# Kernel tuning notes

Measured on AMD Instinct MI355X. Metric: run time of the kernel, lower is better.

Reference implementation:

```python
import jax, jax.numpy as jnp
import numpy as np
import math

N_EMBD = 1024
N_HEAD = 16
N_LAYER = 12


def setup_inputs() -> dict:
    key = jax.random.key(0)
    kx, kw, kb = jax.random.split(key, 3)
    B, T, C = 4, 2048, N_EMBD
    x = jax.random.normal(kx, (B, T, C), dtype=jnp.float32)
    # nn.Linear(C, 3C): weight [3C, C] scaled by 1/sqrt(2*n_layer), bias [3C]
    bound = 1.0 / math.sqrt(C)
    W = jax.random.uniform(kw, (3 * C, C), minval=-bound, maxval=bound, dtype=jnp.float32)
    W = W * (1.0 / math.sqrt(N_LAYER * 2))
    b = jax.random.uniform(kb, (3 * C,), minval=-bound, maxval=bound, dtype=jnp.float32)
    return {"x": x, "W": W, "b": b}


def reference(x, W, b) -> jnp.ndarray:
    B, T, C = x.shape
    H = N_HEAD
    D = C // H
    qkv = jnp.einsum("btc,oc->bto", x, W) + b  # [B, T, 3C]
    q, k, v = jnp.split(qkv, 3, axis=-1)
    # [B, H, T, D]
    q = q.reshape(B, T, H, D).transpose(0, 2, 1, 3)
    k = k.reshape(B, T, H, D).transpose(0, 2, 1, 3)
    v = v.reshape(B, T, H, D).transpose(0, 2, 1, 3)
    att = jnp.einsum("bhtd,bhsd->bhts", q, k) / math.sqrt(D)  # [B, H, T, T]
    causal = jnp.tril(jnp.ones((T, T), dtype=bool))
    att = jnp.where(causal, att, -jnp.inf)
    att = jax.nn.softmax(att, axis=-1)
    y = jnp.einsum("bhts,bhsd->bhtd", att, v)  # [B, H, T, D]
    return y.transpose(0, 2, 1, 3).reshape(B, T, C)
```

## Files before the change

kernel.cpp:

```cpp
#include <hip/hip_runtime.h>


typedef __attribute__((ext_vector_type(8))) short short8;
typedef __attribute__((ext_vector_type(4))) short s16x4;
typedef __attribute__((ext_vector_type(4))) float f32x4;

#define AS1 __attribute__((address_space(1)))
#define AS3 __attribute__((address_space(3)))

__device__ __forceinline__ unsigned short f2bf(float f) {
  unsigned int u = __float_as_uint(f);
  u += 0x7fffu + ((u >> 16) & 1u);
  return (unsigned short)(u >> 16);
}

__device__ __forceinline__ unsigned int pack_bf16(float lo, float hi) {
  return __builtin_amdgcn_perm(__float_as_uint(hi) + 0x8000u,
                               __float_as_uint(lo) + 0x8000u, 0x07060302u);
}

__device__ __forceinline__ void async_copy16(const unsigned short* g, unsigned short* l) {
  const AS1 unsigned char* gp = (const AS1 unsigned char*)(unsigned long long)(uintptr_t)g;
  AS3 unsigned char* lp = (AS3 unsigned char*)(unsigned int)(uintptr_t)l;
  __builtin_amdgcn_global_load_lds((const AS1 void*)gp, (AS3 void*)lp, 16, 0, 0);
}

__global__ __launch_bounds__(256) void cvt_both(const float* __restrict__ x,
                                                const float* __restrict__ W,
                                                unsigned short* __restrict__ xt,
                                                unsigned short* __restrict__ wt) {
  int U = blockIdx.x * 256 + threadIdx.x;
  const float* in;
  unsigned short* out;
  if (U < 1048576) { in = x; out = xt; }
  else             { in = W; out = wt; U -= 1048576; }
  int u6 = U & 63, frag = (U >> 6) & 15, kt = (U >> 10) & 15, bt = U >> 14;
  int ks = frag & 1, i = (frag >> 1) & 3, half = frag >> 3;
  int row = bt * 128 + half * 64 + i * 16 + (u6 & 15);
  int colf = kt * 64 + ks * 32 + (u6 >> 4) * 8;
  const float4* p = (const float4*)(in + (size_t)row * 1024 + colf);
  float4 a = p[0], b = p[1];
  uint4 o;
  o.x = pack_bf16(a.x, a.y);
  o.y = pack_bf16(a.z, a.w);
  o.z = pack_bf16(b.x, b.y);
  o.w = pack_bf16(b.z, b.w);
  *(uint4*)(out + (size_t)U * 8) = o;
}

__global__ __launch_bounds__(256) void qkv_gemm(const unsigned short* __restrict__ xt,
                                                const unsigned short* __restrict__ wt,
                                                const float* __restrict__ bias,
                                                unsigned short* __restrict__ qb,
                                                unsigned short* __restrict__ kvb) {
  __shared__ unsigned short As[2][4096];
  __shared__ unsigned short Bs[2][4096];
  int tid = threadIdx.x;
  int wave = tid >> 6, lane = tid & 63;
  int q4 = lane >> 4, l16 = lane & 15;
  int bm = blockIdx.x, bn = blockIdx.y;

  f32x4 zero = {0.f, 0.f, 0.f, 0.f};
  f32x4 acc[4][4];
#pragma unroll
  for (int i = 0; i < 4; ++i)
#pragma unroll
    for (int j = 0; j < 4; ++j) acc[i][j] = zero;

  const unsigned short* Abase = xt + (size_t)bm * 16 * 8192;
  const unsigned short* Bbase = wt + (size_t)bn * 16 * 8192;

  auto stage = [&](int d, int kt32) {
    int kt64 = kt32 >> 1, ks = kt32 & 1;
    const unsigned short* ga = Abase + (size_t)kt64 * 8192;
    const unsigned short* gb = Bbase + (size_t)kt64 * 8192;
#pragma unroll
    for (int j = 0; j < 2; ++j) {
      int fi = wave * 2 + j;
      int f = (fi >> 2) * 8 + (fi & 3) * 2 + ks;
      async_copy16(ga + f * 512 + lane * 8, &As[d][fi * 512]);
      async_copy16(gb + f * 512 + lane * 8, &Bs[d][fi * 512]);
    }
  };

  stage(0, 0);
  for (int kt = 0; kt < 32; ++kt) {
    __syncthreads();
    if (kt < 31) stage((kt + 1) & 1, kt + 1);
    const unsigned short* Ac = As[kt & 1];
    const unsigned short* Bc = Bs[kt & 1];
    short8 af[4], bf[4];
#pragma unroll
    for (int i = 0; i < 4; ++i)
      af[i] = *(const short8*)(Ac + ((wave & 1) * 4 + i) * 512 + lane * 8);
#pragma unroll
    for (int j = 0; j < 4; ++j)
      bf[j] = *(const short8*)(Bc + ((wave >> 1) * 4 + j) * 512 + lane * 8);
#pragma unroll
    for (int i = 0; i < 4; ++i)
#pragma unroll
      for (int j = 0; j < 4; ++j)
        acc[i][j] = __builtin_amdgcn_mfma_f32_16x16x32_bf16(af[i], bf[j], acc[i][j], 0, 0, 0);
  }

  const float QSCALE = 0.18033688011112042f;
  int rowbase = bm * 128 + (wave & 1) * 64;
  int colbase = bn * 128 + (wave >> 1) * 64;
#pragma unroll
  for (int j = 0; j < 4; ++j) {
    int o = colbase + j * 16 + l16;
    float bv = bias[o];
#pragma unroll
    for (int i = 0; i < 4; ++i) {
      int r0 = rowbase + i * 16 + q4 * 4;
      int b = r0 >> 11, t0 = r0 & 2047;
      if (o < 1024) {
        int h = o >> 6, d = o & 63;
#pragma unroll
        for (int r = 0; r < 4; ++r)
          qb[((((size_t)b * 16 + h) * 2048 + t0 + r) << 6) + d] =
              f2bf((acc[i][j][r] + bv) * QSCALE);
      } else if (o < 2048) {
        int o2 = o - 1024;
        int h = o2 >> 6, dd = o2 & 63;
        int st = t0 >> 6, s6 = t0 & 63;
        int ns = s6 >> 4, l16p = s6 & 15;
        int ks = dd >> 5, q4p = (dd & 31) >> 3, jj = dd & 7;
        size_t base = ((size_t)(b * 16 + h) * 32 + st) * 8192 +
                      ((ns * 2 + ks) * 64 + q4p * 16 + l16p) * 8 + jj;
#pragma unroll
        for (int r = 0; r < 4; ++r)
          kvb[base + r * 8] = f2bf(acc[i][j][r] + bv);
      } else {
        int o3 = o - 2048;
        int h = o3 >> 6, dd = o3 & 63;
        int st = t0 >> 6, s6 = t0 & 63;
        int ns = s6 >> 4, q4p = (s6 >> 2) & 3;
        int p = dd >> 5, halfd = (dd >> 4) & 1, l16p = dd & 15;
        size_t base = ((size_t)(b * 16 + h) * 32 + st) * 8192 + 4096 +
                      ((ns * 2 + p) * 64 + q4p * 16 + l16p) * 8 + halfd * 4;
        ushort4 pk;
        pk.x = f2bf(acc[i][j][0] + bv);
        pk.y = f2bf(acc[i][j][1] + bv);
        pk.z = f2bf(acc[i][j][2] + bv);
        pk.w = f2bf(acc[i][j][3] + bv);
        *(ushort4*)(&kvb[base]) = pk;
      }
    }
  }
}

__global__ __launch_bounds__(128, 4) void flash_attn(const unsigned short* __restrict__ qb,
                                                     const unsigned short* __restrict__ kvb,
                                                     float* __restrict__ out) {
  __shared__ unsigned short buf[2][8192];

  const int tid = threadIdx.x;
  const int wave = tid >> 6, lane = tid & 63;
  const int q4 = lane >> 4, l16 = lane & 15;
  const int n = blockIdx.x;
  const int bh = (n & 7) * 8 + ((n >> 3) & 7);
  const int bx = n >> 6;
  const int b = bh >> 4, h = bh & 15;

  const unsigned short* Qg = qb + (size_t)bh * (2048 * 64);
  const unsigned short* KVg = kvb + (size_t)bh * 32 * 8192;
  const s16x4 ones = {(short)0x3F80, (short)0x3F80, (short)0x3F80, (short)0x3F80};

  auto stage = [&](int d, int st) {
    const unsigned short* tp = KVg + (size_t)st * 8192;
#pragma unroll
    for (int i2 = 0; i2 < 8; ++i2) {
      int u = i2 * 128 + wave * 64;
      async_copy16(tp + (u + lane) * 8, &buf[d][u * 8]);
    }
  };

  for (int pass = 0; pass < 2; ++pass) {
    const int qt = pass ? 31 - bx : bx;
    const int t0w = qt * 64 + wave * 32;

    short8 qf[2][2];
#pragma unroll
    for (int mt = 0; mt < 2; ++mt)
#pragma unroll
      for (int ks = 0; ks < 2; ++ks)
        qf[mt][ks] = *(const short8*)(Qg + (size_t)(t0w + mt * 16 + l16) * 64 +
                                      ks * 32 + q4 * 8);

    f32x4 zero = {0.f, 0.f, 0.f, 0.f};
    f32x4 oT[2][4];
#pragma unroll
    for (int mt = 0; mt < 2; ++mt)
#pragma unroll
      for (int nd = 0; nd < 4; ++nd) oT[mt][nd] = zero;
    f32x4 l_acc[2] = {zero, zero};

    __syncthreads();
    stage(0, 0);
    for (int st = 0; st <= qt; ++st) {
      __syncthreads();
      if (st < qt) stage((st + 1) & 1, st + 1);
      const unsigned short* cur = buf[st & 1];

      f32x4 sT[2][4];
#pragma unroll
      for (int ns = 0; ns < 4; ++ns) {
        short8 kf0 = *(const short8*)(cur + (ns * 2 + 0) * 512 + lane * 8);
        short8 kf1 = *(const short8*)(cur + (ns * 2 + 1) * 512 + lane * 8);
#pragma unroll
        for (int mt = 0; mt < 2; ++mt) {
          sT[mt][ns] = __builtin_amdgcn_mfma_f32_16x16x32_bf16(kf0, qf[mt][0], zero, 0, 0, 0);
          sT[mt][ns] = __builtin_amdgcn_mfma_f32_16x16x32_bf16(kf1, qf[mt][1], sT[mt][ns], 0, 0, 0);
        }
      }

      if (st == qt) {
#pragma unroll
        for (int mt = 0; mt < 2; ++mt) {
          int tg = t0w + mt * 16 + l16;
#pragma unroll
          for (int ns = 0; ns < 4; ++ns) {
            int sgb = st * 64 + ns * 16 + q4 * 4;
#pragma unroll
            for (int r = 0; r < 4; ++r)
              if (sgb + r > tg) sT[mt][ns][r] = -3.0e38f;
          }
        }
      }

#pragma unroll
      for (int ns = 0; ns < 4; ++ns) {
        s16x4 pf[2];
#pragma unroll
        for (int mt = 0; mt < 2; ++mt) {
          union { unsigned int u[2]; s16x4 s4; } pu;
          pu.u[0] = pack_bf16(__builtin_amdgcn_exp2f(sT[mt][ns][0]),
                              __builtin_amdgcn_exp2f(sT[mt][ns][1]));
          pu.u[1] = pack_bf16(__builtin_amdgcn_exp2f(sT[mt][ns][2]),
                              __builtin_amdgcn_exp2f(sT[mt][ns][3]));
          pf[mt] = pu.s4;
        }
#pragma unroll
        for (int p = 0; p < 2; ++p) {
          short8 v8 = *(const short8*)(cur + 4096 + ((ns * 2 + p) * 64 + lane) * 8);
          s16x4 vlo = __builtin_shufflevector(v8, v8, 0, 1, 2, 3);
          s16x4 vhi = __builtin_shufflevector(v8, v8, 4, 5, 6, 7);
#pragma unroll
          for (int mt = 0; mt < 2; ++mt) {
            oT[mt][2 * p] = __builtin_amdgcn_mfma_f32_16x16x16bf16_1k(vlo, pf[mt], oT[mt][2 * p], 0, 0, 0);
            oT[mt][2 * p + 1] = __builtin_amdgcn_mfma_f32_16x16x16bf16_1k(vhi, pf[mt], oT[mt][2 * p + 1], 0, 0, 0);
          }
        }
#pragma unroll
        for (int mt = 0; mt < 2; ++mt)
          l_acc[mt] = __builtin_amdgcn_mfma_f32_16x16x16bf16_1k(ones, pf[mt], l_acc[mt], 0, 0, 0);
      }
    }

#pragma unroll
    for (int mt = 0; mt < 2; ++mt) {
      float inv = 1.0f / l_acc[mt][0];
      int t = t0w + mt * 16 + l16;
      float* op = out + (size_t)(b * 2048 + t) * 1024 + h * 64 + q4 * 4;
#pragma unroll
      for (int nd = 0; nd < 4; ++nd) {
        float4 o4 = {oT[mt][nd][0] * inv, oT[mt][nd][1] * inv,
                     oT[mt][nd][2] * inv, oT[mt][nd][3] * inv};
        *(float4*)(op + nd * 16) = o4;
      }
    }
  }
}

extern "C" void kernel_launch(void* const* d_in, const int* in_sizes, int n_in,
                              void* d_out, int out_size, void* d_ws, size_t ws_size,
                              hipStream_t stream) {
  const float* x = (const float*)d_in[0];
  const float* W = (const float*)d_in[1];
  const float* bias = (const float*)d_in[2];
  float* out = (float*)d_out;

  char* ws = (char*)d_ws;
  unsigned short* xt = (unsigned short*)(ws);
  unsigned short* wt = (unsigned short*)(ws + 16777216);
  unsigned short* qb = (unsigned short*)(ws + 23068672);
  unsigned short* kvb = (unsigned short*)(ws + 39845888);

  hipLaunchKernelGGL(cvt_both, dim3(5632), dim3(256), 0, stream, x, W, xt, wt);
  hipLaunchKernelGGL(qkv_gemm, dim3(64, 24), dim3(256), 0, stream, xt, wt, bias,
                     qb, kvb);
  hipLaunchKernelGGL(flash_attn, dim3(1024), dim3(128), 0, stream, qb, kvb, out);
}
```

Before: 204.2 us.

## Stage bf16 conversion through LDS and reorder tiles so GEMM loads are contiguous

The conversion kernel now has each block convert a 128x64 fp32 tile into LDS with coalesced row reads, then write it out in a new fragment order where each k32 slice is contiguous. The GEMM's async staging uses that order, so each k-step reads a contiguous 8 KB chunk with simple pointer arithmetic instead of strided fragment addressing. This targets poorly coalesced global reads in the conversion and address overhead in the GEMM loads, at the cost of an LDS round trip and a barrier in the conversion.

```diff
diff --git a/kernel.cpp b/kernel.cpp
--- a/kernel.cpp
+++ b/kernel.cpp
@@ -29,23 +29,41 @@
                                                 const float* __restrict__ W,
                                                 unsigned short* __restrict__ xt,
                                                 unsigned short* __restrict__ wt) {
-  int U = blockIdx.x * 256 + threadIdx.x;
+  __shared__ unsigned short lds[128 * 72];
+  const int tid = threadIdx.x;
+  int blk = blockIdx.x;
   const float* in;
-  unsigned short* out;
-  if (U < 1048576) { in = x; out = xt; }
-  else             { in = W; out = wt; U -= 1048576; }
-  int u6 = U & 63, frag = (U >> 6) & 15, kt = (U >> 10) & 15, bt = U >> 14;
-  int ks = frag & 1, i = (frag >> 1) & 3, half = frag >> 3;
-  int row = bt * 128 + half * 64 + i * 16 + (u6 & 15);
-  int colf = kt * 64 + ks * 32 + (u6 >> 4) * 8;
-  const float4* p = (const float4*)(in + (size_t)row * 1024 + colf);
-  float4 a = p[0], b = p[1];
-  uint4 o;
-  o.x = pack_bf16(a.x, a.y);
-  o.y = pack_bf16(a.z, a.w);
-  o.z = pack_bf16(b.x, b.y);
-  o.w = pack_bf16(b.z, b.w);
-  *(uint4*)(out + (size_t)U * 8) = o;
+  unsigned short* outp;
+  int bt, kt;
+  if (blk < 1024) { in = x; outp = xt; bt = blk >> 4; kt = blk & 15; }
+  else { blk -= 1024; in = W; outp = wt; bt = blk >> 4; kt = blk & 15; }
+  const float* src = in + (size_t)(bt * 128) * 1024 + kt * 64;
+  unsigned short* dst = outp + (size_t)(bt * 16 + kt) * 8192;
+
+  const int prow = tid >> 3, pcol = (tid & 7) * 8;
+#pragma unroll
+  for (int step = 0; step < 4; ++step) {
+    int row = step * 32 + prow;
+    const float4* p = (const float4*)(src + (size_t)row * 1024 + pcol);
+    float4 a = p[0], b = p[1];
+    uint4 o;
+    o.x = pack_bf16(a.x, a.y);
+    o.y = pack_bf16(a.z, a.w);
+    o.z = pack_bf16(b.x, b.y);
+    o.w = pack_bf16(b.z, b.w);
+    *(uint4*)(&lds[row * 72 + pcol]) = o;
+  }
+  __syncthreads();
+
+#pragma unroll
+  for (int u = 0; u < 4; ++u) {
+    int U = u * 256 + tid;
+    int ks = U >> 9, slot = (U >> 6) & 7, u6 = U & 63;
+    int srow = (slot >> 2) * 64 + (slot & 3) * 16 + (u6 & 15);
+    int scol = ks * 32 + (u6 >> 4) * 8;
+    uint4 v = *(const uint4*)(&lds[srow * 72 + scol]);
+    *(uint4*)(dst + U * 8) = v;
+  }
 }
 
 __global__ __launch_bounds__(256) void qkv_gemm(const unsigned short* __restrict__ xt,
@@ -67,20 +85,17 @@
 #pragma unroll
     for (int j = 0; j < 4; ++j) acc[i][j] = zero;
 
-  const unsigned short* Abase = xt + (size_t)bm * 16 * 8192;
-  const unsigned short* Bbase = wt + (size_t)bn * 16 * 8192;
+  const unsigned short* ga0 = xt + (size_t)bm * 16 * 8192 + (wave * 2) * 512 + lane * 8;
+  const unsigned short* gb0 = wt + (size_t)bn * 16 * 8192 + (wave * 2) * 512 + lane * 8;
 
   auto stage = [&](int d, int kt32) {
-    int kt64 = kt32 >> 1, ks = kt32 & 1;
-    const unsigned short* ga = Abase + (size_t)kt64 * 8192;
-    const unsigned short* gb = Bbase + (size_t)kt64 * 8192;
-#pragma unroll
-    for (int j = 0; j < 2; ++j) {
-      int fi = wave * 2 + j;
-      int f = (fi >> 2) * 8 + (fi & 3) * 2 + ks;
-      async_copy16(ga + f * 512 + lane * 8, &As[d][fi * 512]);
-      async_copy16(gb + f * 512 + lane * 8, &Bs[d][fi * 512]);
-    }
+    const unsigned short* ga = ga0 + kt32 * 4096;
+    const unsigned short* gb = gb0 + kt32 * 4096;
+    int fb = wave * 2 * 512;
+    async_copy16(ga, &As[d][fb]);
+    async_copy16(ga + 512, &As[d][fb + 512]);
+    async_copy16(gb, &Bs[d][fb]);
+    async_copy16(gb + 512, &Bs[d][fb + 512]);
   };
 
   stage(0, 0);
@@ -287,7 +302,7 @@
   unsigned short* qb = (unsigned short*)(ws + 23068672);
   unsigned short* kvb = (unsigned short*)(ws + 39845888);
 
-  hipLaunchKernelGGL(cvt_both, dim3(5632), dim3(256), 0, stream, x, W, xt, wt);
+  hipLaunchKernelGGL(cvt_both, dim3(1408), dim3(256), 0, stream, x, W, xt, wt);
   hipLaunchKernelGGL(qkv_gemm, dim3(64, 24), dim3(256), 0, stream, xt, wt, bias,
                      qb, kvb);
   hipLaunchKernelGGL(flash_attn, dim3(1024), dim3(128), 0, stream, qb, kvb, out);
```

Result: no change. 206.9 us (+1.3%).
